# Kernel optimization log

Hardware: AMD Instinct MI355X
Metric: run time of the kernel (lower is better)

Reference implementation:

```python
import jax, jax.numpy as jnp
import numpy as np

N = 50000      # nodes
E = 800000     # edges
D_IN = 300     # input node feature dim
D_H = 96       # hidden dim
D_OUT = 2      # classes
G = 64         # graphs in batch


def setup_inputs() -> dict:
    key = jax.random.key(0)
    ks = jax.random.split(key, 10)
    x = jax.random.normal(ks[0], (N, D_IN), dtype=jnp.float32)
    src = jax.random.randint(ks[1], (E,), 0, N, dtype=jnp.int32)
    dst = jax.random.randint(ks[2], (E,), 0, N, dtype=jnp.int32)
    batch = jnp.sort(jax.random.randint(ks[3], (N,), 0, G, dtype=jnp.int32))
    # GCNConv: linear weight (no bias in lin), separate additive bias (PyG default)
    W1 = jax.random.normal(ks[4], (D_IN, D_H), jnp.float32) / np.sqrt(D_IN)
    b1 = jnp.zeros((D_H,), jnp.float32)
    W2 = jax.random.normal(ks[5], (D_H, D_H), jnp.float32) / np.sqrt(D_H)
    b2 = jnp.zeros((D_H,), jnp.float32)
    Wfc = jax.random.normal(ks[6], (D_H, D_OUT), jnp.float32) / np.sqrt(D_H)
    bfc = jnp.zeros((D_OUT,), jnp.float32)
    return {"x": x, "W1": W1, "b1": b1, "W2": W2, "b2": b2,
            "Wfc": Wfc, "bfc": bfc, "src": src, "dst": dst, "batch": batch}


def _gcn_conv(h_in, W, b, src, dst, deg_inv_sqrt):
    """PyG GCNConv with self-loops: out = D^-1/2 (A+I) D^-1/2 (h W) + b."""
    h = h_in @ W                                   # [N, F] transform first
    norm = deg_inv_sqrt[src] * deg_inv_sqrt[dst]   # [E]
    msg = h[src] * norm[:, None]                   # gather + scale (dominant traffic)
    agg = jax.ops.segment_sum(msg, dst, num_segments=N)
    agg = agg + h * (deg_inv_sqrt * deg_inv_sqrt)[:, None]  # self-loop term
    return agg + b


def reference(x, W1, b1, W2, b2, Wfc, bfc, src, dst, batch):
    # degree with self loops, computed on destination nodes (PyG convention)
    deg = jax.ops.segment_sum(jnp.ones((E,), x.dtype), dst, num_segments=N) + 1.0
    dis = jax.lax.rsqrt(deg)
    h = jax.nn.relu(_gcn_conv(x, W1, b1, src, dst, dis))   # dropout = identity (eval)
    h = jax.nn.relu(_gcn_conv(h, W2, b2, src, dst, dis))
    # global mean pool over per-graph node segments
    counts = jax.ops.segment_sum(jnp.ones((N,), x.dtype), batch, num_segments=G)
    pooled = jax.ops.segment_sum(h, batch, num_segments=G) / jnp.maximum(counts, 1.0)[:, None]
    return pooled @ Wfc + bfc                               # [G, D_OUT]
```

## Files before the change

kernel.cpp:

```cpp
#include <hip/hip_runtime.h>
#include <hip/hip_bf16.h>

#define NN 50000
#define NE 800000
#define DIN 300
#define KP1 320
#define DH 96
#define DOUTC 2
#define NG 64

#define NKB 10
#define NFRAG (NKB * 6 * 64)

#define DSTRIDE 64
#define NB1 ((NN + 63) / 64)
#define EPB 1024

typedef __attribute__((ext_vector_type(8))) short bf16x8;
typedef __attribute__((ext_vector_type(4))) float f32x4;

__device__ inline unsigned short f2bf(float f) {
    unsigned int u = __float_as_uint(f);
    unsigned int r = (u + 0x7fffu + ((u >> 16) & 1u)) >> 16;
    return (unsigned short)r;
}
__device__ inline float b2f(unsigned short u) {
    return __uint_as_float((unsigned int)u << 16);
}

__global__ void k_prep(int* cnt, float* pooled,
                       const float* __restrict__ W1, unsigned short* __restrict__ wt1f,
                       const float* __restrict__ W2, unsigned short* __restrict__ wt2) {
    int i = blockIdx.x * blockDim.x + threadIdx.x;
    if (i < NN) cnt[i] = 0;
    if (i < NG * DH) pooled[i] = 0.f;
    if (i < NFRAG * 8) {
        int j = i & 7;
        int f = i >> 3;
        int lane = f & 63;
        int ft = f >> 6;
        int t = ft % 6;
        int kb = ft / 6;
        int row = (lane & 15) + 16 * t;
        int col = kb * 32 + (lane >> 4) * 8 + j;
        wt1f[i] = (col < DIN) ? f2bf(W1[(size_t)col * DH + row]) : (unsigned short)0;
    }
    if (i < DH * DH) {
        int j = i / DH, k = i - j * DH;
        wt2[i] = f2bf(W2[(size_t)k * DH + j]);
    }
}

__global__ void k_dis(const int* __restrict__ cnt, float* __restrict__ dis) {
    int i = blockIdx.x * blockDim.x + threadIdx.x;
    if (i < NN) dis[i] = rsqrtf(1.0f + (float)cnt[i]);
}

__global__ __launch_bounds__(256) void k_gemm1s(const float* __restrict__ A,
        const unsigned short* __restrict__ WF, unsigned short* __restrict__ Cb,
        const int* __restrict__ src, const int* __restrict__ dst,
        int* cnt, unsigned short* __restrict__ esrc) {
    __shared__ unsigned short ldsB[NFRAG * 8];
    const int tid = threadIdx.x;
    {
        const uint4* srcv = (const uint4*)WF;
        uint4* dstv = (uint4*)ldsB;
        #pragma unroll
        for (int f = 0; f < NFRAG / 256; ++f)
            dstv[f * 256 + tid] = srcv[f * 256 + tid];
    }
    __syncthreads();

    const int wv = tid >> 6;
    const int lane = tid & 63;
    const int m = lane & 15;
    const int quad = lane >> 4;
    const int row = blockIdx.x * 64 + wv * 16 + m;
    const int arow = row < NN ? row : NN - 1;
    const float* ap = A + (size_t)arow * DIN + quad * 8;
    const float4 z4 = make_float4(0.f, 0.f, 0.f, 0.f);
    const bf16x8* lb = (const bf16x8*)ldsB;
    f32x4 acc[6];
    #pragma unroll
    for (int t = 0; t < 6; ++t) acc[t] = (f32x4){0.f, 0.f, 0.f, 0.f};

    float4 pa[4][2];
    #pragma unroll
    for (int i = 0; i < 3; ++i) {
        int kb = i * 32 + quad * 8;
        pa[i][0] = (kb + 4 <= DIN) ? *(const float4*)(ap + i * 32) : z4;
        pa[i][1] = (kb + 8 <= DIN) ? *(const float4*)(ap + i * 32 + 4) : z4;
    }

    #pragma unroll
    for (int i = 0; i < NKB; ++i) {
        if (i + 3 < NKB) {
            int kb = (i + 3) * 32 + quad * 8;
            pa[(i + 3) & 3][0] = (kb + 4 <= DIN) ? *(const float4*)(ap + (i + 3) * 32) : z4;
            pa[(i + 3) & 3][1] = (kb + 8 <= DIN) ? *(const float4*)(ap + (i + 3) * 32 + 4) : z4;
        }
        float4 a0 = pa[i & 3][0], a1 = pa[i & 3][1];
        bf16x8 af;
        af[0] = (short)f2bf(a0.x); af[1] = (short)f2bf(a0.y);
        af[2] = (short)f2bf(a0.z); af[3] = (short)f2bf(a0.w);
        af[4] = (short)f2bf(a1.x); af[5] = (short)f2bf(a1.y);
        af[6] = (short)f2bf(a1.z); af[7] = (short)f2bf(a1.w);
        #pragma unroll
        for (int t = 0; t < 6; ++t) {
            bf16x8 bf = lb[(i * 6 + t) * 64 + lane];
            acc[t] = __builtin_amdgcn_mfma_f32_16x16x32_bf16(af, bf, acc[t], 0, 0, 0);
        }
    }
    const int rbase = blockIdx.x * 64 + wv * 16 + quad * 4;
    #pragma unroll
    for (int r = 0; r < 4; ++r) {
        int rr = rbase + r;
        if (rr < NN) {
            unsigned short* cp = Cb + (size_t)rr * DH + m;
            #pragma unroll
            for (int t = 0; t < 6; ++t) cp[t * 16] = f2bf(acc[t][r]);
        }
    }

    const int ebase = blockIdx.x * EPB;
    #pragma unroll
    for (int k = 0; k < EPB / 256; ++k) {
        int e = ebase + k * 256 + tid;
        if (e < NE) {
            int d = dst[e];
            int pos = atomicAdd(&cnt[d], 1);
            if (pos < DSTRIDE) esrc[(size_t)d * DSTRIDE + pos] = (unsigned short)src[e];
        }
    }
}

__global__ __launch_bounds__(256) void k_gemm2(const unsigned short* __restrict__ Ab,
        const unsigned short* __restrict__ WT, unsigned short* __restrict__ Cb) {
    const int tid = threadIdx.x;
    const int wv = tid >> 6;
    const int lane = tid & 63;
    const int m = lane & 15;
    const int quad = lane >> 4;
    const int row = blockIdx.x * 64 + wv * 16 + m;
    const int arow = row < NN ? row : NN - 1;
    const unsigned short* ap = Ab + (size_t)arow * DH + quad * 8;
    const unsigned short* wp = WT + (size_t)m * DH + quad * 8;
    bf16x8 af[3], bf[3][6];
    #pragma unroll
    for (int i = 0; i < 3; ++i) af[i] = *(const bf16x8*)(ap + i * 32);
    #pragma unroll
    for (int i = 0; i < 3; ++i)
        #pragma unroll
        for (int t = 0; t < 6; ++t)
            bf[i][t] = *(const bf16x8*)(wp + (size_t)t * 16 * DH + i * 32);
    f32x4 acc[6];
    #pragma unroll
    for (int t = 0; t < 6; ++t) acc[t] = (f32x4){0.f, 0.f, 0.f, 0.f};
    #pragma unroll
    for (int i = 0; i < 3; ++i)
        #pragma unroll
        for (int t = 0; t < 6; ++t)
            acc[t] = __builtin_amdgcn_mfma_f32_16x16x32_bf16(af[i], bf[i][t], acc[t], 0, 0, 0);
    const int rbase = blockIdx.x * 64 + wv * 16 + quad * 4;
    #pragma unroll
    for (int r = 0; r < 4; ++r) {
        int rr = rbase + r;
        if (rr < NN) {
            unsigned short* cp = Cb + (size_t)rr * DH + m;
            #pragma unroll
            for (int t = 0; t < 6; ++t) cp[t * 16] = f2bf(acc[t][r]);
        }
    }
}

#define QH (DH / 4)
template <bool BFOUT>
__global__ void k_agg(const ushort4* __restrict__ hb, const float* __restrict__ dis,
                      const int* __restrict__ cnt,
                      const unsigned short* __restrict__ esrc,
                      const float4* __restrict__ bias4, float4* __restrict__ fout,
                      ushort4* __restrict__ bout) {
    int gid = blockIdx.x * blockDim.x + threadIdx.x;
    if (gid >= NN * QH) return;
    int n = gid / QH;
    int q = gid - n * QH;
    int count = cnt[n];
    if (count > DSTRIDE) count = DSTRIDE;
    const int beg = n * DSTRIDE;
    const int end = beg + count;
    float dn = dis[n];
    ushort4 u0 = hb[(size_t)n * QH + q];
    float4 acc = make_float4(dn * b2f(u0.x), dn * b2f(u0.y), dn * b2f(u0.z), dn * b2f(u0.w));
    int e = beg;
    for (; e + 3 < end; e += 4) {
        int s0 = esrc[e], s1 = esrc[e + 1], s2 = esrc[e + 2], s3 = esrc[e + 3];
        float d0 = dis[s0], d1 = dis[s1], d2 = dis[s2], d3 = dis[s3];
        ushort4 v0 = hb[(size_t)s0 * QH + q];
        ushort4 v1 = hb[(size_t)s1 * QH + q];
        ushort4 v2 = hb[(size_t)s2 * QH + q];
        ushort4 v3 = hb[(size_t)s3 * QH + q];
        acc.x = fmaf(d0, b2f(v0.x), acc.x); acc.y = fmaf(d0, b2f(v0.y), acc.y);
        acc.z = fmaf(d0, b2f(v0.z), acc.z); acc.w = fmaf(d0, b2f(v0.w), acc.w);
        acc.x = fmaf(d1, b2f(v1.x), acc.x); acc.y = fmaf(d1, b2f(v1.y), acc.y);
        acc.z = fmaf(d1, b2f(v1.z), acc.z); acc.w = fmaf(d1, b2f(v1.w), acc.w);
        acc.x = fmaf(d2, b2f(v2.x), acc.x); acc.y = fmaf(d2, b2f(v2.y), acc.y);
        acc.z = fmaf(d2, b2f(v2.z), acc.z); acc.w = fmaf(d2, b2f(v2.w), acc.w);
        acc.x = fmaf(d3, b2f(v3.x), acc.x); acc.y = fmaf(d3, b2f(v3.y), acc.y);
        acc.z = fmaf(d3, b2f(v3.z), acc.z); acc.w = fmaf(d3, b2f(v3.w), acc.w);
    }
    for (; e < end; ++e) {
        int s = esrc[e];
        float ds = dis[s];
        ushort4 v = hb[(size_t)s * QH + q];
        acc.x = fmaf(ds, b2f(v.x), acc.x);
        acc.y = fmaf(ds, b2f(v.y), acc.y);
        acc.z = fmaf(ds, b2f(v.z), acc.z);
        acc.w = fmaf(ds, b2f(v.w), acc.w);
    }
    float4 b = bias4[q];
    float4 r;
    r.x = fmaxf(fmaf(dn, acc.x, b.x), 0.f);
    r.y = fmaxf(fmaf(dn, acc.y, b.y), 0.f);
    r.z = fmaxf(fmaf(dn, acc.z, b.z), 0.f);
    r.w = fmaxf(fmaf(dn, acc.w, b.w), 0.f);
    if (BFOUT) {
        ushort4 o;
        o.x = f2bf(r.x); o.y = f2bf(r.y); o.z = f2bf(r.z); o.w = f2bf(r.w);
        bout[gid] = o;
    } else {
        fout[gid] = r;
    }
}

#define PNODES 32
__global__ void k_pool_partial(const float* __restrict__ h, const int* __restrict__ batch,
                               float* __restrict__ pooled) {
    __shared__ int sbatch[PNODES];
    const int n0 = blockIdx.x * PNODES;
    const int nend = min(n0 + PNODES, NN);
    const int cnt = nend - n0;
    const int f = threadIdx.x;
    if (f < cnt) sbatch[f] = batch[n0 + f];
    __syncthreads();
    if (f < DH) {
        float acc = 0.f;
        int cur = sbatch[0];
        for (int i = 0; i < cnt; ++i) {
            int g = sbatch[i];
            if (g != cur) {
                atomicAdd(&pooled[cur * DH + f], acc);
                acc = 0.f; cur = g;
            }
            acc += h[(size_t)(n0 + i) * DH + f];
        }
        atomicAdd(&pooled[cur * DH + f], acc);
    }
}

__global__ void k_fc(const float* __restrict__ pooled, const int* __restrict__ batch,
                     const float* __restrict__ Wfc, const float* __restrict__ bfc,
                     float* __restrict__ out) {
    const int t = threadIdx.x;
    if (t >= NG * DOUTC) return;
    const int g = t / DOUTC;
    const int c = t - g * DOUTC;
    int lo = 0, hi = NN;
    while (lo < hi) { int mid = (lo + hi) >> 1; if (batch[mid] < g) lo = mid + 1; else hi = mid; }
    const int s = lo;
    hi = NN;
    while (lo < hi) { int mid = (lo + hi) >> 1; if (batch[mid] < g + 1) lo = mid + 1; else hi = mid; }
    float inv = 1.f / fmaxf((float)(lo - s), 1.f);
    float acc = bfc[c];
    #pragma unroll 8
    for (int j = 0; j < DH; ++j)
        acc += pooled[g * DH + j] * inv * Wfc[j * DOUTC + c];
    out[g * DOUTC + c] = acc;
}

extern "C" void kernel_launch(void* const* d_in, const int* in_sizes, int n_in,
                              void* d_out, int out_size, void* d_ws, size_t ws_size,
                              hipStream_t stream) {
    const float* x   = (const float*)d_in[0];
    const float* W1  = (const float*)d_in[1];
    const float* b1  = (const float*)d_in[2];
    const float* W2  = (const float*)d_in[3];
    const float* b2  = (const float*)d_in[4];
    const float* Wfc = (const float*)d_in[5];
    const float* bfc = (const float*)d_in[6];
    const int* src   = (const int*)d_in[7];
    const int* dst   = (const int*)d_in[8];
    const int* batch = (const int*)d_in[9];
    float* out = (float*)d_out;

    unsigned short* hb  = (unsigned short*)d_ws;
    unsigned short* a1b = hb + (size_t)NN * DH;
    float* hbuf  = (float*)(a1b + (size_t)NN * DH);
    float* dis   = hbuf + (size_t)NN * DH;
    float* pooled= dis + NN;
    int* cnt     = (int*)(pooled + NG * DH);
    unsigned short* esrc = (unsigned short*)(cnt + NN);
    unsigned short* wt1f = esrc + (size_t)NN * DSTRIDE;
    unsigned short* wt2  = wt1f + NFRAG * 8;

    const int TB = 256;
    k_prep<<<(NN + TB - 1) / TB, TB, 0, stream>>>(cnt, pooled, W1, wt1f, W2, wt2);
    k_gemm1s<<<NB1, 256, 0, stream>>>(x, wt1f, hb, src, dst, cnt, esrc);
    k_dis<<<(NN + TB - 1) / TB, TB, 0, stream>>>(cnt, dis);
    k_agg<true><<<(NN * QH + TB - 1) / TB, TB, 0, stream>>>(
        (const ushort4*)hb, dis, cnt, esrc, (const float4*)b1,
        nullptr, (ushort4*)a1b);
    k_gemm2<<<NB1, 256, 0, stream>>>(a1b, wt2, hb);
    k_agg<false><<<(NN * QH + TB - 1) / TB, TB, 0, stream>>>(
        (const ushort4*)hb, dis, cnt, esrc, (const float4*)b2,
        (float4*)hbuf, nullptr);
    k_pool_partial<<<(NN + PNODES - 1) / PNODES, 128, 0, stream>>>(hbuf, batch, pooled);
    k_fc<<<1, 128, 0, stream>>>(pooled, batch, Wfc, bfc, out);
}
```

Before: 270.7 us.

## Split GEMM1 and edge scatter across alternating blocks, inline degree rsqrt

The fused GEMM1/edge-bucketing kernel now launches twice as many blocks. Odd blocks only do the edge scatter, using vectorized int4 loads of src/dst, and even blocks only do the GEMM tile, so the two workloads run concurrently instead of serially within each block. The separate k_dis kernel and the dis buffer are removed. Aggregation now recomputes rsqrt(1+cnt) from the count array for each neighbor, trading an extra rsqrt per gather for one fewer launch and less memory traffic.

```diff
diff --git a/kernel.cpp b/kernel.cpp
--- a/kernel.cpp
+++ b/kernel.cpp
@@ -51,17 +51,37 @@
     }
 }
 
-__global__ void k_dis(const int* __restrict__ cnt, float* __restrict__ dis) {
-    int i = blockIdx.x * blockDim.x + threadIdx.x;
-    if (i < NN) dis[i] = rsqrtf(1.0f + (float)cnt[i]);
-}
-
-__global__ __launch_bounds__(256) void k_gemm1s(const float* __restrict__ A,
+__global__ __launch_bounds__(256) void k_g1sc(const float* __restrict__ A,
         const unsigned short* __restrict__ WF, unsigned short* __restrict__ Cb,
         const int* __restrict__ src, const int* __restrict__ dst,
         int* cnt, unsigned short* __restrict__ esrc) {
     __shared__ unsigned short ldsB[NFRAG * 8];
     const int tid = threadIdx.x;
+
+    if (blockIdx.x & 1) {
+        const int ebase = (blockIdx.x >> 1) * EPB + tid * 4;
+        if (ebase + 3 < NE) {
+            int4 d4 = *(const int4*)&dst[ebase];
+            int4 s4 = *(const int4*)&src[ebase];
+            int p0 = atomicAdd(&cnt[d4.x], 1);
+            int p1 = atomicAdd(&cnt[d4.y], 1);
+            int p2 = atomicAdd(&cnt[d4.z], 1);
+            int p3 = atomicAdd(&cnt[d4.w], 1);
+            if (p0 < DSTRIDE) esrc[(size_t)d4.x * DSTRIDE + p0] = (unsigned short)s4.x;
+            if (p1 < DSTRIDE) esrc[(size_t)d4.y * DSTRIDE + p1] = (unsigned short)s4.y;
+            if (p2 < DSTRIDE) esrc[(size_t)d4.z * DSTRIDE + p2] = (unsigned short)s4.z;
+            if (p3 < DSTRIDE) esrc[(size_t)d4.w * DSTRIDE + p3] = (unsigned short)s4.w;
+        } else {
+            for (int e = ebase; e < NE; ++e) {
+                int d = dst[e];
+                int pos = atomicAdd(&cnt[d], 1);
+                if (pos < DSTRIDE) esrc[(size_t)d * DSTRIDE + pos] = (unsigned short)src[e];
+            }
+        }
+        return;
+    }
+
+    const int tile = blockIdx.x >> 1;
     {
         const uint4* srcv = (const uint4*)WF;
         uint4* dstv = (uint4*)ldsB;
@@ -75,7 +95,7 @@
     const int lane = tid & 63;
     const int m = lane & 15;
     const int quad = lane >> 4;
-    const int row = blockIdx.x * 64 + wv * 16 + m;
+    const int row = tile * 64 + wv * 16 + m;
     const int arow = row < NN ? row : NN - 1;
     const float* ap = A + (size_t)arow * DIN + quad * 8;
     const float4 z4 = make_float4(0.f, 0.f, 0.f, 0.f);
@@ -111,7 +131,7 @@
             acc[t] = __builtin_amdgcn_mfma_f32_16x16x32_bf16(af, bf, acc[t], 0, 0, 0);
         }
     }
-    const int rbase = blockIdx.x * 64 + wv * 16 + quad * 4;
+    const int rbase = tile * 64 + wv * 16 + quad * 4;
     #pragma unroll
     for (int r = 0; r < 4; ++r) {
         int rr = rbase + r;
@@ -119,17 +139,6 @@
             unsigned short* cp = Cb + (size_t)rr * DH + m;
             #pragma unroll
             for (int t = 0; t < 6; ++t) cp[t * 16] = f2bf(acc[t][r]);
-        }
-    }
-
-    const int ebase = blockIdx.x * EPB;
-    #pragma unroll
-    for (int k = 0; k < EPB / 256; ++k) {
-        int e = ebase + k * 256 + tid;
-        if (e < NE) {
-            int d = dst[e];
-            int pos = atomicAdd(&cnt[d], 1);
-            if (pos < DSTRIDE) esrc[(size_t)d * DSTRIDE + pos] = (unsigned short)src[e];
         }
     }
 }
@@ -175,7 +184,7 @@
 
 #define QH (DH / 4)
 template <bool BFOUT>
-__global__ void k_agg(const ushort4* __restrict__ hb, const float* __restrict__ dis,
+__global__ void k_agg(const ushort4* __restrict__ hb,
                       const int* __restrict__ cnt,
                       const unsigned short* __restrict__ esrc,
                       const float4* __restrict__ bias4, float4* __restrict__ fout,
@@ -185,16 +194,19 @@
     int n = gid / QH;
     int q = gid - n * QH;
     int count = cnt[n];
+    float dn = rsqrtf(1.0f + (float)count);
     if (count > DSTRIDE) count = DSTRIDE;
     const int beg = n * DSTRIDE;
     const int end = beg + count;
-    float dn = dis[n];
     ushort4 u0 = hb[(size_t)n * QH + q];
     float4 acc = make_float4(dn * b2f(u0.x), dn * b2f(u0.y), dn * b2f(u0.z), dn * b2f(u0.w));
     int e = beg;
     for (; e + 3 < end; e += 4) {
         int s0 = esrc[e], s1 = esrc[e + 1], s2 = esrc[e + 2], s3 = esrc[e + 3];
-        float d0 = dis[s0], d1 = dis[s1], d2 = dis[s2], d3 = dis[s3];
+        float d0 = rsqrtf(1.0f + (float)cnt[s0]);
+        float d1 = rsqrtf(1.0f + (float)cnt[s1]);
+        float d2 = rsqrtf(1.0f + (float)cnt[s2]);
+        float d3 = rsqrtf(1.0f + (float)cnt[s3]);
         ushort4 v0 = hb[(size_t)s0 * QH + q];
         ushort4 v1 = hb[(size_t)s1 * QH + q];
         ushort4 v2 = hb[(size_t)s2 * QH + q];
@@ -210,7 +222,7 @@
     }
     for (; e < end; ++e) {
         int s = esrc[e];
-        float ds = dis[s];
+        float ds = rsqrtf(1.0f + (float)cnt[s]);
         ushort4 v = hb[(size_t)s * QH + q];
         acc.x = fmaf(ds, b2f(v.x), acc.x);
         acc.y = fmaf(ds, b2f(v.y), acc.y);
@@ -295,8 +307,7 @@
     unsigned short* hb  = (unsigned short*)d_ws;
     unsigned short* a1b = hb + (size_t)NN * DH;
     float* hbuf  = (float*)(a1b + (size_t)NN * DH);
-    float* dis   = hbuf + (size_t)NN * DH;
-    float* pooled= dis + NN;
+    float* pooled= hbuf + (size_t)NN * DH;
     int* cnt     = (int*)(pooled + NG * DH);
     unsigned short* esrc = (unsigned short*)(cnt + NN);
     unsigned short* wt1f = esrc + (size_t)NN * DSTRIDE;
@@ -304,14 +315,13 @@
 
     const int TB = 256;
     k_prep<<<(NN + TB - 1) / TB, TB, 0, stream>>>(cnt, pooled, W1, wt1f, W2, wt2);
-    k_gemm1s<<<NB1, 256, 0, stream>>>(x, wt1f, hb, src, dst, cnt, esrc);
-    k_dis<<<(NN + TB - 1) / TB, TB, 0, stream>>>(cnt, dis);
+    k_g1sc<<<NB1 * 2, 256, 0, stream>>>(x, wt1f, hb, src, dst, cnt, esrc);
     k_agg<true><<<(NN * QH + TB - 1) / TB, TB, 0, stream>>>(
-        (const ushort4*)hb, dis, cnt, esrc, (const float4*)b1,
+        (const ushort4*)hb, cnt, esrc, (const float4*)b1,
         nullptr, (ushort4*)a1b);
     k_gemm2<<<NB1, 256, 0, stream>>>(a1b, wt2, hb);
     k_agg<false><<<(NN * QH + TB - 1) / TB, TB, 0, stream>>>(
-        (const ushort4*)hb, dis, cnt, esrc, (const float4*)b2,
+        (const ushort4*)hb, cnt, esrc, (const float4*)b2,
         (float4*)hbuf, nullptr);
     k_pool_partial<<<(NN + PNODES - 1) / PNODES, 128, 0, stream>>>(hbuf, batch, pooled);
     k_fc<<<1, 128, 0, stream>>>(pooled, batch, Wfc, bfc, out);
```

New measurement: 243.6 us. 1.11x faster.
